# Performance work log

Hardware: AMD Instinct MI355X
Metric: run time of the kernel (lower is better)

## Reference

```python
import jax, jax.numpy as jnp
import numpy as np


def setup_inputs() -> dict:
    key = jax.random.key(0)
    k1, k2 = jax.random.split(key)
    N, H, CH, T = 4, 8, 64, 2048
    q = jax.random.normal(k1, (N, H * CH, T), dtype=jnp.float32)
    kv = jax.random.normal(k2, (N, H * 2 * CH, T), dtype=jnp.float32)
    return {"q": q, "kv": kv, "n_heads": H}


def reference(q, kv, n_heads):
    # q: [N, H*C, T], kv: [N, H*2C, T]
    N, q_width, T = q.shape
    width = kv.shape[1]
    ch = (q_width + width) // (3 * n_heads)
    qh = q.reshape(N * n_heads, ch, T)
    k, v = jnp.split(kv.reshape(N * n_heads, 2 * ch, T), 2, axis=1)
    scale = 1.0 / (ch ** 0.25)  # applied to both q and k -> total 1/sqrt(ch)
    weight = jnp.einsum('bct,bcs->bts', qh * scale, k * scale)  # [B*H, T, T]
    weight = jax.nn.softmax(weight.astype(jnp.float32), axis=-1).astype(weight.dtype)
    a = jnp.einsum('bts,bcs->bct', weight, v)  # [B*H, ch, T]
    return a.reshape(N, -1, T)
```

## Files before the change

kernel.cpp:

```cpp
#include <hip/hip_runtime.h>
#include <hip/hip_bf16.h>

#define T_DIM 2048
#define CH    64
#define TQ    256
#define TS    64
#define PITCH 72
#define NTHREADS 1024
#define NIT   (T_DIM / TS)

typedef __attribute__((ext_vector_type(8)))  short bf16x8;
typedef __attribute__((ext_vector_type(4)))  short bf16x4;
typedef __attribute__((ext_vector_type(16))) float f32x16;

__device__ __forceinline__ f32x16 mfma32(bf16x8 a, bf16x8 b, f32x16 c) {
    return __builtin_amdgcn_mfma_f32_32x32x16_bf16(a, b, c, 0, 0, 0);
}
__device__ __forceinline__ short f2bf(float x) {
    __hip_bfloat16 h = __float2bfloat16(x);
    return *reinterpret_cast<short*>(&h);
}
__device__ __forceinline__ unsigned pk2(float a, float b) {
    return (unsigned)(unsigned short)f2bf(a) | ((unsigned)(unsigned short)f2bf(b) << 16);
}

__global__ __launch_bounds__(NTHREADS, 4)
void attn_fwd(const float* __restrict__ qg, const float* __restrict__ kvg,
              float* __restrict__ outg) {
    const int head = blockIdx.y;
    const int t0   = blockIdx.x * TQ;

    const float* qbase = qg  + (size_t)head * CH * T_DIM + t0;
    const float* kbase = kvg + (size_t)head * 2 * CH * T_DIM;
    const float* vbase = kbase + (size_t)CH * T_DIM;
    float*       obase = outg + (size_t)head * CH * T_DIM + t0;

    __shared__ alignas(16) __hip_bfloat16 kvsm[2 * 2 * TS * PITCH];
    __hip_bfloat16 (*Kt)[TS][PITCH] = reinterpret_cast<__hip_bfloat16 (*)[TS][PITCH]>(kvsm);
    __hip_bfloat16 (*Vs)[TS][PITCH] = reinterpret_cast<__hip_bfloat16 (*)[TS][PITCH]>(kvsm + 2 * TS * PITCH);
    __shared__ alignas(16) float eps[8][64][33];
    __shared__ float lsm[8][32];
    __hip_bfloat16 (*Qt)[PITCH] = reinterpret_cast<__hip_bfloat16 (*)[PITCH]>(&eps[0][0][0]);

    const int tid  = threadIdx.x;
    const int w    = tid >> 6;
    const int ws   = w & 7;
    const int sh   = w >> 3;
    const int l    = tid & 63;
    const int lr32 = l & 31;
    const int hi   = l >> 5;
    const int tb0  = 32 * ws;

    const float qscale = 0.125f * 1.44269504089f;

    const int kc4 = (tid & 15) * 4;
    const int ks2 = (tid >> 4) * 2;
    const int vu  = tid & 511;
    const int vc  = vu >> 3;
    const int vs8 = (vu & 7) * 8;

    float2 kp[4];
    float4 vp[2];

    if (tid < 512) {
        #pragma unroll
        for (int cc = 0; cc < 4; ++cc)
            kp[cc] = *reinterpret_cast<const float2*>(kbase + (kc4 + cc) * T_DIM + ks2);
    } else {
        const float* vpp = vbase + (size_t)vc * T_DIM + vs8;
        vp[0] = *reinterpret_cast<const float4*>(vpp);
        vp[1] = *reinterpret_cast<const float4*>(vpp + 4);
    }

    {
        const int c8 = (tid & 7) * 8;
        const int t2 = (tid >> 3) * 2;
        bf16x8 r0, r1;
        #pragma unroll
        for (int cc = 0; cc < 8; ++cc) {
            float2 f = *reinterpret_cast<const float2*>(qbase + (c8 + cc) * T_DIM + t2);
            r0[cc] = f2bf(f.x * qscale);
            r1[cc] = f2bf(f.y * qscale);
        }
        *reinterpret_cast<bf16x8*>(&Qt[t2    ][c8]) = r0;
        *reinterpret_cast<bf16x8*>(&Qt[t2 + 1][c8]) = r1;
    }

    if (tid < 512) {
        bf16x4 r0, r1;
        #pragma unroll
        for (int cc = 0; cc < 4; ++cc) { r0[cc] = f2bf(kp[cc].x); r1[cc] = f2bf(kp[cc].y); }
        *reinterpret_cast<bf16x4*>(&Kt[0][ks2    ][kc4]) = r0;
        *reinterpret_cast<bf16x4*>(&Kt[0][ks2 + 1][kc4]) = r1;
    } else {
        bf16x8 r;
        r[0]=f2bf(vp[0].x); r[1]=f2bf(vp[0].y); r[2]=f2bf(vp[0].z); r[3]=f2bf(vp[0].w);
        r[4]=f2bf(vp[1].x); r[5]=f2bf(vp[1].y); r[6]=f2bf(vp[1].z); r[7]=f2bf(vp[1].w);
        *reinterpret_cast<bf16x8*>(&Vs[0][vc][vs8]) = r;
    }
    __syncthreads();

    bf16x8 qf[4];
    #pragma unroll
    for (int kc = 0; kc < 4; ++kc)
        qf[kc] = *reinterpret_cast<const bf16x8*>(&Qt[tb0 + lr32][16 * kc + 8 * hi]);

    f32x16 accO[2];
    #pragma unroll
    for (int cb = 0; cb < 2; ++cb)
        #pragma unroll
        for (int i = 0; i < 16; ++i) accO[cb][i] = 0.f;
    float2 lsum2 = {0.f, 0.f};

    int cur = 0;
    for (int it = 0; it < NIT; ++it) {
        const bool pf = (it + 1 < NIT);

        if (pf) {
            const int s_next = (it + 1) * TS;
            if (tid < 512) {
                #pragma unroll
                for (int cc = 0; cc < 4; ++cc)
                    kp[cc] = *reinterpret_cast<const float2*>(kbase + (kc4 + cc) * T_DIM + s_next + ks2);
            } else {
                const float* vpp = vbase + (size_t)vc * T_DIM + s_next + vs8;
                vp[0] = *reinterpret_cast<const float4*>(vpp);
                vp[1] = *reinterpret_cast<const float4*>(vpp + 4);
            }
        }

        f32x16 accS;
        #pragma unroll
        for (int i = 0; i < 16; ++i) accS[i] = 0.f;
        __builtin_amdgcn_s_setprio(1);
        #pragma unroll
        for (int kc = 0; kc < 4; ++kc) {
            bf16x8 ak = *reinterpret_cast<const bf16x8*>(
                &Kt[cur][32 * sh + lr32][16 * kc + 8 * hi]);
            accS = mfma32(ak, qf[kc], accS);
        }
        __builtin_amdgcn_s_setprio(0);

        unsigned pw[8];
        #pragma unroll
        for (int i = 0; i < 8; ++i) {
            float e0 = __builtin_amdgcn_exp2f(accS[2 * i]);
            float e1 = __builtin_amdgcn_exp2f(accS[2 * i + 1]);
            lsum2.x += e0;
            lsum2.y += e1;
            pw[i] = pk2(e0, e1);
        }

        bf16x8 pb[2];
        #pragma unroll
        for (int f = 0; f < 2; ++f) {
            unsigned a0 = pw[4 * f], b0 = pw[4 * f + 2];
            unsigned a1 = pw[4 * f + 1], b1 = pw[4 * f + 3];
            asm("v_permlane32_swap_b32 %0, %1" : "+v"(a0), "+v"(b0));
            asm("v_permlane32_swap_b32 %0, %1" : "+v"(a1), "+v"(b1));
            union { unsigned u[4]; bf16x8 v; } uu;
            uu.u[0] = a0; uu.u[1] = a1; uu.u[2] = b0; uu.u[3] = b1;
            pb[f] = uu.v;
        }

        __builtin_amdgcn_s_setprio(1);
        #pragma unroll
        for (int f = 0; f < 2; ++f) {
            #pragma unroll
            for (int cb = 0; cb < 2; ++cb) {
                bf16x8 av = *reinterpret_cast<const bf16x8*>(
                    &Vs[cur][32 * cb + lr32][32 * sh + 16 * f + 8 * hi]);
                accO[cb] = mfma32(av, pb[f], accO[cb]);
            }
        }
        __builtin_amdgcn_s_setprio(0);

        if (pf) {
            if (tid < 512) {
                bf16x4 r0, r1;
                #pragma unroll
                for (int cc = 0; cc < 4; ++cc) { r0[cc] = f2bf(kp[cc].x); r1[cc] = f2bf(kp[cc].y); }
                *reinterpret_cast<bf16x4*>(&Kt[cur ^ 1][ks2    ][kc4]) = r0;
                *reinterpret_cast<bf16x4*>(&Kt[cur ^ 1][ks2 + 1][kc4]) = r1;
            } else {
                bf16x8 r;
                r[0]=f2bf(vp[0].x); r[1]=f2bf(vp[0].y); r[2]=f2bf(vp[0].z); r[3]=f2bf(vp[0].w);
                r[4]=f2bf(vp[1].x); r[5]=f2bf(vp[1].y); r[6]=f2bf(vp[1].z); r[7]=f2bf(vp[1].w);
                *reinterpret_cast<bf16x8*>(&Vs[cur ^ 1][vc][vs8]) = r;
            }
        }
        __syncthreads();
        cur ^= 1;
    }

    float lsum = lsum2.x + lsum2.y;
    lsum += __shfl_xor(lsum, 32);

    if (sh == 1) {
        #pragma unroll
        for (int cb = 0; cb < 2; ++cb)
            #pragma unroll
            for (int reg = 0; reg < 16; ++reg) {
                int c = 32 * cb + (reg & 3) + 8 * (reg >> 2) + 4 * hi;
                eps[ws][c][lr32] = accO[cb][reg];
            }
        if (l < 32) lsm[ws][l] = lsum;
    }
    __syncthreads();
    if (sh == 0) {
        const float linv = 1.0f / (lsum + lsm[ws][lr32]);
        const int t = tb0 + lr32;
        #pragma unroll
        for (int cb = 0; cb < 2; ++cb)
            #pragma unroll
            for (int reg = 0; reg < 16; ++reg) {
                int c = 32 * cb + (reg & 3) + 8 * (reg >> 2) + 4 * hi;
                obase[(size_t)c * T_DIM + t] = (accO[cb][reg] + eps[ws][c][lr32]) * linv;
            }
    }
}

extern "C" void kernel_launch(void* const* d_in, const int* in_sizes, int n_in,
                              void* d_out, int out_size, void* d_ws, size_t ws_size,
                              hipStream_t stream) {
    const float* q  = (const float*)d_in[0];
    const float* kv = (const float*)d_in[1];
    float* out = (float*)d_out;
    (void)in_sizes; (void)n_in; (void)out_size; (void)d_ws; (void)ws_size;
    dim3 grid(T_DIM / TQ, 32);
    attn_fwd<<<grid, NTHREADS, 0, stream>>>(q, kv, out);
}
```

Baseline: 62.87 us.

## Halve query tile to 128, use 512 threads, and map heads to XCDs

Shrinks the per-block query tile from 256 to 128 rows and the block from 1024 to 512 threads, which doubles the grid to 512 blocks. The grid becomes 1-D and is remapped so that blocks of the same head land on the same XCD, which should improve L2 reuse of K/V. Shared memory is cut by aliasing Q staging and the epilogue buffer onto the K/V buffer, which adds an extra barrier. Each thread now loads twice as much K/V per iteration, and K/V global traffic doubles overall because every head's keys are streamed by twice as many blocks.

```diff
diff --git a/kernel.cpp b/kernel.cpp
--- a/kernel.cpp
+++ b/kernel.cpp
@@ -3,14 +3,13 @@
 
 #define T_DIM 2048
 #define CH    64
-#define TQ    256
+#define TQ    128
 #define TS    64
 #define PITCH 72
-#define NTHREADS 1024
+#define NTHREADS 512
 #define NIT   (T_DIM / TS)
 
 typedef __attribute__((ext_vector_type(8)))  short bf16x8;
-typedef __attribute__((ext_vector_type(4)))  short bf16x4;
 typedef __attribute__((ext_vector_type(16))) float f32x16;
 
 __device__ __forceinline__ f32x16 mfma32(bf16x8 a, bf16x8 b, f32x16 c) {
@@ -27,8 +26,11 @@
 __global__ __launch_bounds__(NTHREADS, 4)
 void attn_fwd(const float* __restrict__ qg, const float* __restrict__ kvg,
               float* __restrict__ outg) {
-    const int head = blockIdx.y;
-    const int t0   = blockIdx.x * TQ;
+    const int bid  = blockIdx.x;
+    const int xcd  = bid & 7;
+    const int slot = bid >> 3;
+    const int head = xcd + 8 * (slot >> 4);
+    const int t0   = (slot & 15) * TQ;
 
     const float* qbase = qg  + (size_t)head * CH * T_DIM + t0;
     const float* kbase = kvg + (size_t)head * 2 * CH * T_DIM;
@@ -38,14 +40,14 @@
     __shared__ alignas(16) __hip_bfloat16 kvsm[2 * 2 * TS * PITCH];
     __hip_bfloat16 (*Kt)[TS][PITCH] = reinterpret_cast<__hip_bfloat16 (*)[TS][PITCH]>(kvsm);
     __hip_bfloat16 (*Vs)[TS][PITCH] = reinterpret_cast<__hip_bfloat16 (*)[TS][PITCH]>(kvsm + 2 * TS * PITCH);
-    __shared__ alignas(16) float eps[8][64][33];
-    __shared__ float lsm[8][32];
-    __hip_bfloat16 (*Qt)[PITCH] = reinterpret_cast<__hip_bfloat16 (*)[PITCH]>(&eps[0][0][0]);
+    __hip_bfloat16 (*Qt)[PITCH] = reinterpret_cast<__hip_bfloat16 (*)[PITCH]>(kvsm);
+    float (*eps)[64][33] = reinterpret_cast<float (*)[64][33]>(kvsm);
+    __shared__ float lsm[4][32];
 
     const int tid  = threadIdx.x;
     const int w    = tid >> 6;
-    const int ws   = w & 7;
-    const int sh   = w >> 3;
+    const int ws   = w & 3;
+    const int sh   = w >> 2;
     const int l    = tid & 63;
     const int lr32 = l & 31;
     const int hi   = l >> 5;
@@ -53,23 +55,24 @@
 
     const float qscale = 0.125f * 1.44269504089f;
 
-    const int kc4 = (tid & 15) * 4;
-    const int ks2 = (tid >> 4) * 2;
-    const int vu  = tid & 511;
-    const int vc  = vu >> 3;
-    const int vs8 = (vu & 7) * 8;
-
-    float2 kp[4];
-    float4 vp[2];
-
-    if (tid < 512) {
-        #pragma unroll
-        for (int cc = 0; cc < 4; ++cc)
-            kp[cc] = *reinterpret_cast<const float2*>(kbase + (kc4 + cc) * T_DIM + ks2);
+    const int kc8  = (tid & 7) * 8;
+    const int ks2  = (tid >> 3) * 2;
+    const int vu   = tid & 255;
+    const int vc   = vu >> 2;
+    const int vs16 = (vu & 3) * 16;
+
+    float2 kp[8];
+    float4 vp[4];
+
+    if (tid < 256) {
+        #pragma unroll
+        for (int cc = 0; cc < 8; ++cc)
+            kp[cc] = *reinterpret_cast<const float2*>(kbase + (kc8 + cc) * T_DIM + ks2);
     } else {
-        const float* vpp = vbase + (size_t)vc * T_DIM + vs8;
-        vp[0] = *reinterpret_cast<const float4*>(vpp);
-        vp[1] = *reinterpret_cast<const float4*>(vpp + 4);
+        const float* vpp = vbase + (size_t)vc * T_DIM + vs16;
+        #pragma unroll
+        for (int j = 0; j < 4; ++j)
+            vp[j] = *reinterpret_cast<const float4*>(vpp + 4 * j);
     }
 
     {
@@ -85,25 +88,30 @@
         *reinterpret_cast<bf16x8*>(&Qt[t2    ][c8]) = r0;
         *reinterpret_cast<bf16x8*>(&Qt[t2 + 1][c8]) = r1;
     }
-
-    if (tid < 512) {
-        bf16x4 r0, r1;
-        #pragma unroll
-        for (int cc = 0; cc < 4; ++cc) { r0[cc] = f2bf(kp[cc].x); r1[cc] = f2bf(kp[cc].y); }
-        *reinterpret_cast<bf16x4*>(&Kt[0][ks2    ][kc4]) = r0;
-        *reinterpret_cast<bf16x4*>(&Kt[0][ks2 + 1][kc4]) = r1;
-    } else {
-        bf16x8 r;
-        r[0]=f2bf(vp[0].x); r[1]=f2bf(vp[0].y); r[2]=f2bf(vp[0].z); r[3]=f2bf(vp[0].w);
-        r[4]=f2bf(vp[1].x); r[5]=f2bf(vp[1].y); r[6]=f2bf(vp[1].z); r[7]=f2bf(vp[1].w);
-        *reinterpret_cast<bf16x8*>(&Vs[0][vc][vs8]) = r;
-    }
     __syncthreads();
 
     bf16x8 qf[4];
     #pragma unroll
     for (int kc = 0; kc < 4; ++kc)
         qf[kc] = *reinterpret_cast<const bf16x8*>(&Qt[tb0 + lr32][16 * kc + 8 * hi]);
+    __syncthreads();
+
+    if (tid < 256) {
+        bf16x8 r0, r1;
+        #pragma unroll
+        for (int cc = 0; cc < 8; ++cc) { r0[cc] = f2bf(kp[cc].x); r1[cc] = f2bf(kp[cc].y); }
+        *reinterpret_cast<bf16x8*>(&Kt[0][ks2    ][kc8]) = r0;
+        *reinterpret_cast<bf16x8*>(&Kt[0][ks2 + 1][kc8]) = r1;
+    } else {
+        bf16x8 r0, r1;
+        r0[0]=f2bf(vp[0].x); r0[1]=f2bf(vp[0].y); r0[2]=f2bf(vp[0].z); r0[3]=f2bf(vp[0].w);
+        r0[4]=f2bf(vp[1].x); r0[5]=f2bf(vp[1].y); r0[6]=f2bf(vp[1].z); r0[7]=f2bf(vp[1].w);
+        r1[0]=f2bf(vp[2].x); r1[1]=f2bf(vp[2].y); r1[2]=f2bf(vp[2].z); r1[3]=f2bf(vp[2].w);
+        r1[4]=f2bf(vp[3].x); r1[5]=f2bf(vp[3].y); r1[6]=f2bf(vp[3].z); r1[7]=f2bf(vp[3].w);
+        *reinterpret_cast<bf16x8*>(&Vs[0][vc][vs16    ]) = r0;
+        *reinterpret_cast<bf16x8*>(&Vs[0][vc][vs16 + 8]) = r1;
+    }
+    __syncthreads();
 
     f32x16 accO[2];
     #pragma unroll
@@ -118,14 +126,15 @@
 
         if (pf) {
             const int s_next = (it + 1) * TS;
-            if (tid < 512) {
+            if (tid < 256) {
                 #pragma unroll
-                for (int cc = 0; cc < 4; ++cc)
-                    kp[cc] = *reinterpret_cast<const float2*>(kbase + (kc4 + cc) * T_DIM + s_next + ks2);
+                for (int cc = 0; cc < 8; ++cc)
+                    kp[cc] = *reinterpret_cast<const float2*>(kbase + (kc8 + cc) * T_DIM + s_next + ks2);
             } else {
-                const float* vpp = vbase + (size_t)vc * T_DIM + s_next + vs8;
-                vp[0] = *reinterpret_cast<const float4*>(vpp);
-                vp[1] = *reinterpret_cast<const float4*>(vpp + 4);
+                const float* vpp = vbase + (size_t)vc * T_DIM + s_next + vs16;
+                #pragma unroll
+                for (int j = 0; j < 4; ++j)
+                    vp[j] = *reinterpret_cast<const float4*>(vpp + 4 * j);
             }
         }
 
@@ -176,17 +185,20 @@
         __builtin_amdgcn_s_setprio(0);
 
         if (pf) {
-            if (tid < 512) {
-                bf16x4 r0, r1;
+            if (tid < 256) {
+                bf16x8 r0, r1;
                 #pragma unroll
-                for (int cc = 0; cc < 4; ++cc) { r0[cc] = f2bf(kp[cc].x); r1[cc] = f2bf(kp[cc].y); }
-                *reinterpret_cast<bf16x4*>(&Kt[cur ^ 1][ks2    ][kc4]) = r0;
-                *reinterpret_cast<bf16x4*>(&Kt[cur ^ 1][ks2 + 1][kc4]) = r1;
+                for (int cc = 0; cc < 8; ++cc) { r0[cc] = f2bf(kp[cc].x); r1[cc] = f2bf(kp[cc].y); }
+                *reinterpret_cast<bf16x8*>(&Kt[cur ^ 1][ks2    ][kc8]) = r0;
+                *reinterpret_cast<bf16x8*>(&Kt[cur ^ 1][ks2 + 1][kc8]) = r1;
             } else {
-                bf16x8 r;
-                r[0]=f2bf(vp[0].x); r[1]=f2bf(vp[0].y); r[2]=f2bf(vp[0].z); r[3]=f2bf(vp[0].w);
-                r[4]=f2bf(vp[1].x); r[5]=f2bf(vp[1].y); r[6]=f2bf(vp[1].z); r[7]=f2bf(vp[1].w);
-                *reinterpret_cast<bf16x8*>(&Vs[cur ^ 1][vc][vs8]) = r;
+                bf16x8 r0, r1;
+                r0[0]=f2bf(vp[0].x); r0[1]=f2bf(vp[0].y); r0[2]=f2bf(vp[0].z); r0[3]=f2bf(vp[0].w);
+                r0[4]=f2bf(vp[1].x); r0[5]=f2bf(vp[1].y); r0[6]=f2bf(vp[1].z); r0[7]=f2bf(vp[1].w);
+                r1[0]=f2bf(vp[2].x); r1[1]=f2bf(vp[2].y); r1[2]=f2bf(vp[2].z); r1[3]=f2bf(vp[2].w);
+                r1[4]=f2bf(vp[3].x); r1[5]=f2bf(vp[3].y); r1[6]=f2bf(vp[3].z); r1[7]=f2bf(vp[3].w);
+                *reinterpret_cast<bf16x8*>(&Vs[cur ^ 1][vc][vs16    ]) = r0;
+                *reinterpret_cast<bf16x8*>(&Vs[cur ^ 1][vc][vs16 + 8]) = r1;
             }
         }
         __syncthreads();
@@ -227,6 +239,5 @@
     const float* kv = (const float*)d_in[1];
     float* out = (float*)d_out;
     (void)in_sizes; (void)n_in; (void)out_size; (void)d_ws; (void)ws_size;
-    dim3 grid(T_DIM / TQ, 32);
-    attn_fwd<<<grid, NTHREADS, 0, stream>>>(q, kv, out);
-}
+    attn_fwd<<<dim3(512), NTHREADS, 0, stream>>>(q, kv, out);
+}
```

After: 110.3 us. 75.4% more time.

## Double KV tile size per iteration and remap blocks so heads share an XCD

Applied to the files above, without the earlier changes.

Raises the key/value tile from 64 to 128 positions per loop step, which halves the number of barriers and global-load rounds. Each wave now processes two 32-row sub-blocks per step, and V gets its own padded layout. The launch becomes a 1D grid whose block index is decoded so that all query tiles of one head land on the same XCD, which should improve L2 reuse of K/V. In exchange it uses more registers and LDS, and launch bounds drop to 2 blocks per CU, so occupancy falls.

```diff
diff --git a/kernel.cpp b/kernel.cpp
--- a/kernel.cpp
+++ b/kernel.cpp
@@ -4,10 +4,14 @@
 #define T_DIM 2048
 #define CH    64
 #define TQ    256
-#define TS    64
-#define PITCH 72
+#define TS    128
+#define KP    72
+#define VP    136
 #define NTHREADS 1024
 #define NIT   (T_DIM / TS)
+
+#define KBYTES (2 * TS * KP * 2)
+#define VBYTES (2 * CH * VP * 2)
 
 typedef __attribute__((ext_vector_type(8)))  short bf16x8;
 typedef __attribute__((ext_vector_type(4)))  short bf16x4;
@@ -24,23 +28,27 @@
     return (unsigned)(unsigned short)f2bf(a) | ((unsigned)(unsigned short)f2bf(b) << 16);
 }
 
-__global__ __launch_bounds__(NTHREADS, 4)
+__global__ __launch_bounds__(NTHREADS, 2)
 void attn_fwd(const float* __restrict__ qg, const float* __restrict__ kvg,
               float* __restrict__ outg) {
-    const int head = blockIdx.y;
-    const int t0   = blockIdx.x * TQ;
+    const int bid  = blockIdx.x;
+    const int xcd  = bid & 7;
+    const int slot = bid >> 3;
+    const int head = xcd + 8 * (slot >> 3);
+    const int tt   = slot & 7;
+    const int t0   = tt * TQ;
 
     const float* qbase = qg  + (size_t)head * CH * T_DIM + t0;
     const float* kbase = kvg + (size_t)head * 2 * CH * T_DIM;
     const float* vbase = kbase + (size_t)CH * T_DIM;
     float*       obase = outg + (size_t)head * CH * T_DIM + t0;
 
-    __shared__ alignas(16) __hip_bfloat16 kvsm[2 * 2 * TS * PITCH];
-    __hip_bfloat16 (*Kt)[TS][PITCH] = reinterpret_cast<__hip_bfloat16 (*)[TS][PITCH]>(kvsm);
-    __hip_bfloat16 (*Vs)[TS][PITCH] = reinterpret_cast<__hip_bfloat16 (*)[TS][PITCH]>(kvsm + 2 * TS * PITCH);
-    __shared__ alignas(16) float eps[8][64][33];
+    __shared__ alignas(16) char sm[KBYTES + VBYTES];
+    __hip_bfloat16 (*Kt)[TS][KP] = reinterpret_cast<__hip_bfloat16 (*)[TS][KP]>(sm);
+    __hip_bfloat16 (*Vs)[CH][VP] = reinterpret_cast<__hip_bfloat16 (*)[CH][VP]>(sm + KBYTES);
+    __hip_bfloat16 (*Qt)[KP]     = reinterpret_cast<__hip_bfloat16 (*)[KP]>(sm);
+    float (*eps)[64][33]         = reinterpret_cast<float (*)[64][33]>(sm);
     __shared__ float lsm[8][32];
-    __hip_bfloat16 (*Qt)[PITCH] = reinterpret_cast<__hip_bfloat16 (*)[PITCH]>(&eps[0][0][0]);
 
     const int tid  = threadIdx.x;
     const int w    = tid >> 6;
@@ -59,17 +67,21 @@
     const int vc  = vu >> 3;
     const int vs8 = (vu & 7) * 8;
 
-    float2 kp[4];
-    float4 vp[2];
+    float2 kpA[4], kpB[4];
+    float4 vpA[2], vpB[2];
 
     if (tid < 512) {
         #pragma unroll
-        for (int cc = 0; cc < 4; ++cc)
-            kp[cc] = *reinterpret_cast<const float2*>(kbase + (kc4 + cc) * T_DIM + ks2);
+        for (int cc = 0; cc < 4; ++cc) {
+            kpA[cc] = *reinterpret_cast<const float2*>(kbase + (kc4 + cc) * T_DIM + ks2);
+            kpB[cc] = *reinterpret_cast<const float2*>(kbase + (kc4 + cc) * T_DIM + 64 + ks2);
+        }
     } else {
         const float* vpp = vbase + (size_t)vc * T_DIM + vs8;
-        vp[0] = *reinterpret_cast<const float4*>(vpp);
-        vp[1] = *reinterpret_cast<const float4*>(vpp + 4);
+        vpA[0] = *reinterpret_cast<const float4*>(vpp);
+        vpA[1] = *reinterpret_cast<const float4*>(vpp + 4);
+        vpB[0] = *reinterpret_cast<const float4*>(vpp + 64);
+        vpB[1] = *reinterpret_cast<const float4*>(vpp + 68);
     }
 
     {
@@ -85,25 +97,35 @@
         *reinterpret_cast<bf16x8*>(&Qt[t2    ][c8]) = r0;
         *reinterpret_cast<bf16x8*>(&Qt[t2 + 1][c8]) = r1;
     }
-
-    if (tid < 512) {
-        bf16x4 r0, r1;
-        #pragma unroll
-        for (int cc = 0; cc < 4; ++cc) { r0[cc] = f2bf(kp[cc].x); r1[cc] = f2bf(kp[cc].y); }
-        *reinterpret_cast<bf16x4*>(&Kt[0][ks2    ][kc4]) = r0;
-        *reinterpret_cast<bf16x4*>(&Kt[0][ks2 + 1][kc4]) = r1;
-    } else {
-        bf16x8 r;
-        r[0]=f2bf(vp[0].x); r[1]=f2bf(vp[0].y); r[2]=f2bf(vp[0].z); r[3]=f2bf(vp[0].w);
-        r[4]=f2bf(vp[1].x); r[5]=f2bf(vp[1].y); r[6]=f2bf(vp[1].z); r[7]=f2bf(vp[1].w);
-        *reinterpret_cast<bf16x8*>(&Vs[0][vc][vs8]) = r;
-    }
     __syncthreads();
 
     bf16x8 qf[4];
     #pragma unroll
     for (int kc = 0; kc < 4; ++kc)
         qf[kc] = *reinterpret_cast<const bf16x8*>(&Qt[tb0 + lr32][16 * kc + 8 * hi]);
+    __syncthreads();
+
+    if (tid < 512) {
+        #pragma unroll
+        for (int h = 0; h < 2; ++h) {
+            const float2* kp = h ? kpB : kpA;
+            bf16x4 r0, r1;
+            #pragma unroll
+            for (int cc = 0; cc < 4; ++cc) { r0[cc] = f2bf(kp[cc].x); r1[cc] = f2bf(kp[cc].y); }
+            *reinterpret_cast<bf16x4*>(&Kt[0][64 * h + ks2    ][kc4]) = r0;
+            *reinterpret_cast<bf16x4*>(&Kt[0][64 * h + ks2 + 1][kc4]) = r1;
+        }
+    } else {
+        #pragma unroll
+        for (int h = 0; h < 2; ++h) {
+            const float4* vp = h ? vpB : vpA;
+            bf16x8 r;
+            r[0]=f2bf(vp[0].x); r[1]=f2bf(vp[0].y); r[2]=f2bf(vp[0].z); r[3]=f2bf(vp[0].w);
+            r[4]=f2bf(vp[1].x); r[5]=f2bf(vp[1].y); r[6]=f2bf(vp[1].z); r[7]=f2bf(vp[1].w);
+            *reinterpret_cast<bf16x8*>(&Vs[0][vc][64 * h + vs8]) = r;
+        }
+    }
+    __syncthreads();
 
     f32x16 accO[2];
     #pragma unroll
@@ -117,76 +139,92 @@
         const bool pf = (it + 1 < NIT);
 
         if (pf) {
-            const int s_next = (it + 1) * TS;
+            const int sn = (it + 1) * TS;
             if (tid < 512) {
                 #pragma unroll
-                for (int cc = 0; cc < 4; ++cc)
-                    kp[cc] = *reinterpret_cast<const float2*>(kbase + (kc4 + cc) * T_DIM + s_next + ks2);
+                for (int cc = 0; cc < 4; ++cc) {
+                    kpA[cc] = *reinterpret_cast<const float2*>(kbase + (kc4 + cc) * T_DIM + sn + ks2);
+                    kpB[cc] = *reinterpret_cast<const float2*>(kbase + (kc4 + cc) * T_DIM + sn + 64 + ks2);
+                }
             } else {
-                const float* vpp = vbase + (size_t)vc * T_DIM + s_next + vs8;
-                vp[0] = *reinterpret_cast<const float4*>(vpp);
-                vp[1] = *reinterpret_cast<const float4*>(vpp + 4);
-            }
-        }
-
-        f32x16 accS;
-        #pragma unroll
-        for (int i = 0; i < 16; ++i) accS[i] = 0.f;
-        __builtin_amdgcn_s_setprio(1);
-        #pragma unroll
-        for (int kc = 0; kc < 4; ++kc) {
-            bf16x8 ak = *reinterpret_cast<const bf16x8*>(
-                &Kt[cur][32 * sh + lr32][16 * kc + 8 * hi]);
-            accS = mfma32(ak, qf[kc], accS);
-        }
-        __builtin_amdgcn_s_setprio(0);
-
-        unsigned pw[8];
-        #pragma unroll
-        for (int i = 0; i < 8; ++i) {
-            float e0 = __builtin_amdgcn_exp2f(accS[2 * i]);
-            float e1 = __builtin_amdgcn_exp2f(accS[2 * i + 1]);
-            lsum2.x += e0;
-            lsum2.y += e1;
-            pw[i] = pk2(e0, e1);
-        }
-
-        bf16x8 pb[2];
-        #pragma unroll
-        for (int f = 0; f < 2; ++f) {
-            unsigned a0 = pw[4 * f], b0 = pw[4 * f + 2];
-            unsigned a1 = pw[4 * f + 1], b1 = pw[4 * f + 3];
-            asm("v_permlane32_swap_b32 %0, %1" : "+v"(a0), "+v"(b0));
-            asm("v_permlane32_swap_b32 %0, %1" : "+v"(a1), "+v"(b1));
-            union { unsigned u[4]; bf16x8 v; } uu;
-            uu.u[0] = a0; uu.u[1] = a1; uu.u[2] = b0; uu.u[3] = b1;
-            pb[f] = uu.v;
-        }
-
-        __builtin_amdgcn_s_setprio(1);
-        #pragma unroll
-        for (int f = 0; f < 2; ++f) {
-            #pragma unroll
-            for (int cb = 0; cb < 2; ++cb) {
-                bf16x8 av = *reinterpret_cast<const bf16x8*>(
-                    &Vs[cur][32 * cb + lr32][32 * sh + 16 * f + 8 * hi]);
-                accO[cb] = mfma32(av, pb[f], accO[cb]);
-            }
-        }
-        __builtin_amdgcn_s_setprio(0);
+                const float* vpp = vbase + (size_t)vc * T_DIM + sn + vs8;
+                vpA[0] = *reinterpret_cast<const float4*>(vpp);
+                vpA[1] = *reinterpret_cast<const float4*>(vpp + 4);
+                vpB[0] = *reinterpret_cast<const float4*>(vpp + 64);
+                vpB[1] = *reinterpret_cast<const float4*>(vpp + 68);
+            }
+        }
+
+        #pragma unroll
+        for (int sb2 = 0; sb2 < 2; ++sb2) {
+            const int srow = 64 * sh + 32 * sb2;
+            f32x16 accS;
+            #pragma unroll
+            for (int i = 0; i < 16; ++i) accS[i] = 0.f;
+            __builtin_amdgcn_s_setprio(1);
+            #pragma unroll
+            for (int kc = 0; kc < 4; ++kc) {
+                bf16x8 ak = *reinterpret_cast<const bf16x8*>(
+                    &Kt[cur][srow + lr32][16 * kc + 8 * hi]);
+                accS = mfma32(ak, qf[kc], accS);
+            }
+            __builtin_amdgcn_s_setprio(0);
+
+            unsigned pw[8];
+            #pragma unroll
+            for (int i = 0; i < 8; ++i) {
+                float e0 = __builtin_amdgcn_exp2f(accS[2 * i]);
+                float e1 = __builtin_amdgcn_exp2f(accS[2 * i + 1]);
+                lsum2.x += e0;
+                lsum2.y += e1;
+                pw[i] = pk2(e0, e1);
+            }
+
+            bf16x8 pb[2];
+            #pragma unroll
+            for (int f = 0; f < 2; ++f) {
+                unsigned a0 = pw[4 * f], b0 = pw[4 * f + 2];
+                unsigned a1 = pw[4 * f + 1], b1 = pw[4 * f + 3];
+                asm("v_permlane32_swap_b32 %0, %1" : "+v"(a0), "+v"(b0));
+                asm("v_permlane32_swap_b32 %0, %1" : "+v"(a1), "+v"(b1));
+                union { unsigned u[4]; bf16x8 v; } uu;
+                uu.u[0] = a0; uu.u[1] = a1; uu.u[2] = b0; uu.u[3] = b1;
+                pb[f] = uu.v;
+            }
+
+            __builtin_amdgcn_s_setprio(1);
+            #pragma unroll
+            for (int f = 0; f < 2; ++f) {
+                #pragma unroll
+                for (int cb = 0; cb < 2; ++cb) {
+                    bf16x8 av = *reinterpret_cast<const bf16x8*>(
+                        &Vs[cur][32 * cb + lr32][srow + 16 * f + 8 * hi]);
+                    accO[cb] = mfma32(av, pb[f], accO[cb]);
+                }
+            }
+            __builtin_amdgcn_s_setprio(0);
+        }
 
         if (pf) {
             if (tid < 512) {
-                bf16x4 r0, r1;
-                #pragma unroll
-                for (int cc = 0; cc < 4; ++cc) { r0[cc] = f2bf(kp[cc].x); r1[cc] = f2bf(kp[cc].y); }
-                *reinterpret_cast<bf16x4*>(&Kt[cur ^ 1][ks2    ][kc4]) = r0;
-                *reinterpret_cast<bf16x4*>(&Kt[cur ^ 1][ks2 + 1][kc4]) = r1;
+                #pragma unroll
+                for (int h = 0; h < 2; ++h) {
+                    const float2* kp = h ? kpB : kpA;
+                    bf16x4 r0, r1;
+                    #pragma unroll
+                    for (int cc = 0; cc < 4; ++cc) { r0[cc] = f2bf(kp[cc].x); r1[cc] = f2bf(kp[cc].y); }
+                    *reinterpret_cast<bf16x4*>(&Kt[cur ^ 1][64 * h + ks2    ][kc4]) = r0;
+                    *reinterpret_cast<bf16x4*>(&Kt[cur ^ 1][64 * h + ks2 + 1][kc4]) = r1;
+                }
             } else {
-                bf16x8 r;
-                r[0]=f2bf(vp[0].x); r[1]=f2bf(vp[0].y); r[2]=f2bf(vp[0].z); r[3]=f2bf(vp[0].w);
-                r[4]=f2bf(vp[1].x); r[5]=f2bf(vp[1].y); r[6]=f2bf(vp[1].z); r[7]=f2bf(vp[1].w);
-                *reinterpret_cast<bf16x8*>(&Vs[cur ^ 1][vc][vs8]) = r;
+                #pragma unroll
+                for (int h = 0; h < 2; ++h) {
+                    const float4* vp = h ? vpB : vpA;
+                    bf16x8 r;
+                    r[0]=f2bf(vp[0].x); r[1]=f2bf(vp[0].y); r[2]=f2bf(vp[0].z); r[3]=f2bf(vp[0].w);
+                    r[4]=f2bf(vp[1].x); r[5]=f2bf(vp[1].y); r[6]=f2bf(vp[1].z); r[7]=f2bf(vp[1].w);
+                    *reinterpret_cast<bf16x8*>(&Vs[cur ^ 1][vc][64 * h + vs8]) = r;
+                }
             }
         }
         __syncthreads();
@@ -227,6 +265,5 @@
     const float* kv = (const float*)d_in[1];
     float* out = (float*)d_out;
     (void)in_sizes; (void)n_in; (void)out_size; (void)d_ws; (void)ws_size;
-    dim3 grid(T_DIM / TQ, 32);
-    attn_fwd<<<grid, NTHREADS, 0, stream>>>(q, kv, out);
-}
+    attn_fwd<<<dim3(256), NTHREADS, 0, stream>>>(q, kv, out);
+}
```

New measurement: 75.36 us. 19.9% more time.
